# Performance work log

Hardware: AMD Instinct MI355X
Metric: run time of the kernel (lower is better)

Reference implementation:

```python
import jax, jax.numpy as jnp
import numpy as np

B, N, DIM, H, DH, P = 4, 4096, 256, 8, 64, 2
INNER = H * DH  # 512


def setup_inputs() -> dict:
    key = jax.random.key(0)
    ks = jax.random.split(key, 10)
    w = lambda k, shape: jax.random.normal(k, shape, dtype=jnp.float32) * 0.02
    return dict(
        x=jax.random.normal(ks[0], (B, N, DIM), dtype=jnp.float32),
        prev_x=jax.random.normal(ks[1], (B, N, DIM), dtype=jnp.float32),
        ln_q_g=jnp.ones((2 * DIM,), jnp.float32), ln_q_b=jnp.zeros((2 * DIM,), jnp.float32),
        ln_k_g=jnp.ones((DIM,), jnp.float32), ln_k_b=jnp.zeros((DIM,), jnp.float32),
        ln_v_g=jnp.ones((DIM,), jnp.float32), ln_v_b=jnp.zeros((DIM,), jnp.float32),
        Wq=w(ks[2], (2 * DIM, INNER)),            # to_q, bias=False
        Wk=w(ks[3], (DIM, INNER)), bk=jnp.zeros((INNER,), jnp.float32),
        Wv=w(ks[4], (DIM, INNER)), bv=jnp.zeros((INNER,), jnp.float32),
        Woff=w(ks[5], (H * P, INNER)),            # 1x1 conv == linear over channels
        boff=jax.random.uniform(ks[6], (H * P,), jnp.float32, -1.0, 1.0),
        Wout=w(ks[7], (DIM, INNER)), bout=jnp.zeros((DIM,), jnp.float32),
    )


def _ln(x, g, b):
    m = x.mean(-1, keepdims=True)
    v = ((x - m) ** 2).mean(-1, keepdims=True)
    return (x - m) * jax.lax.rsqrt(v + 1e-5) * g + b


def reference(x, prev_x, ln_q_g, ln_q_b, ln_k_g, ln_k_b, ln_v_g, ln_v_b,
              Wq, Wk, bk, Wv, bv, Woff, boff, Wout, bout):
    scale = DH ** -0.5
    # queries from cat(x, prev_x) along feature dim
    q = _ln(jnp.concatenate([x, prev_x], axis=-1), ln_q_g, ln_q_b) @ Wq  # (B,N,INNER)
    # learned per-head, per-point offsets (1x1 conv over channels)
    offsets = (q @ Woff.T + boff).reshape(B, N, H, P).transpose(0, 2, 3, 1)  # (B,H,P,N)
    # K/V from cat(x, prev_x) along batch dim -> KV length 2N per (b,h)
    kv = jnp.concatenate([x, prev_x], axis=0)  # (2B,N,DIM)
    k = (_ln(kv, ln_k_g, ln_k_b) @ Wk + bk).reshape(2, B, N, H, DH).transpose(1, 3, 4, 0, 2).reshape(B, H, DH, 2 * N)
    v = (_ln(kv, ln_v_g, ln_v_b) @ Wv + bv).reshape(2, B, N, H, DH).transpose(1, 3, 4, 0, 2).reshape(B, H, DH, 2 * N)
    # sampling positions: pos + offset, clamped, truncated to int (matches torch .long())
    pos = jnp.arange(N, dtype=jnp.float32)
    samp = jnp.clip(pos[None, None, None, :] + offsets, 0, 2 * N - 1).astype(jnp.int32)  # (B,H,P,N)
    idx = samp.transpose(0, 1, 3, 2)[:, :, None, :, :]  # (B,H,1,N,P)
    k_s = jnp.take_along_axis(k[:, :, :, None, :], idx, axis=-1)  # (B,H,DH,N,P)
    v_s = jnp.take_along_axis(v[:, :, :, None, :], idx, axis=-1)  # (B,H,DH,N,P)
    qh = q.reshape(B, N, H, DH).transpose(0, 2, 1, 3) * scale     # (B,H,N,DH)
    sim = jnp.einsum('bhnd,bhdnp->bhnp', qh, k_s)                  # (B,H,N,P)
    attn = jax.nn.softmax(sim, axis=-1)
    out = jnp.einsum('bhnp,bhdnp->bhnd', attn, v_s)                # (B,H,N,DH)
    out = out.transpose(0, 2, 1, 3).reshape(B, N, INNER) @ Wout.T + bout  # (B,N,DIM)
    return out, offsets
```

## Files before the change

kernel.cpp:

```cpp
#include <hip/hip_runtime.h>
#include <hip/hip_bf16.h>
#include <math.h>

#define B_    4
#define N_    4096
#define DIM_  256
#define H_    8
#define DH_   64
#define P_    2
#define INNER_ 512
#define BN_   (B_ * N_)
#define KVR_  (2 * BN_)

typedef short v8s  __attribute__((ext_vector_type(8)));
typedef short v4s  __attribute__((ext_vector_type(4)));
typedef float v4f  __attribute__((ext_vector_type(4)));

__device__ __forceinline__ short f2b(float x) {
    __hip_bfloat16 h = __float2bfloat16(x);
    return *reinterpret_cast<short*>(&h);
}
__device__ __forceinline__ float b2f(short s) {
    __hip_bfloat16 h = *reinterpret_cast<__hip_bfloat16*>(&s);
    return __bfloat162float(h);
}

__device__ __forceinline__ void storeC(float* p, float v) { *p = v; }
__device__ __forceinline__ void storeC(__hip_bfloat16* p, float v) { *p = __float2bfloat16(v); }

__global__ void prep_t(const float* __restrict__ W, const float* __restrict__ g,
                       const float* __restrict__ beta, const float* __restrict__ bias_in,
                       short* __restrict__ Wt, float* __restrict__ b2, int K, int N) {
    int n = blockIdx.x, t = threadIdx.x;
    float partial = 0.f;
    for (int k = t; k < K; k += 256) {
        float w = W[k * N + n];
        Wt[(size_t)n * K + k] = f2b(g[k] * w);
        partial += beta[k] * w;
    }
    __shared__ float red[256];
    red[t] = partial;
    __syncthreads();
    for (int s = 128; s > 0; s >>= 1) {
        if (t < s) red[t] += red[t + s];
        __syncthreads();
    }
    if (t == 0) b2[n] = (bias_in ? bias_in[n] : 0.f) + red[0];
}

__global__ void cast_bf16(const float* __restrict__ src, short* __restrict__ dst, int n) {
    int i = blockIdx.x * 256 + threadIdx.x;
    if (i < n) dst[i] = f2b(src[i]);
}

__global__ void wcomb_kernel(const float* __restrict__ Wq, const float* __restrict__ gq,
                             const float* __restrict__ Woff, float* __restrict__ Wcomb) {
    int k = blockIdx.x, t = threadIdx.x;
    int hp = t & 15, jg = t >> 4;
    float p = 0.f;
    for (int j = jg; j < INNER_; j += 16)
        p += Wq[k * INNER_ + j] * Woff[hp * INNER_ + j];
    __shared__ float red[16][17];
    red[jg][hp] = p;
    __syncthreads();
    if (t < 16) {
        float s = 0.f;
        for (int i = 0; i < 16; i++) s += red[i][t];
        Wcomb[k * 16 + t] = gq[k] * s;
    }
}

__global__ void bcomb_kernel(const float* __restrict__ bq2, const float* __restrict__ Woff,
                             const float* __restrict__ boff, float* __restrict__ bcomb) {
    int t = threadIdx.x;
    int hp = t & 15, jg = t >> 4;
    float p = 0.f;
    for (int j = jg; j < INNER_; j += 16)
        p += bq2[j] * Woff[hp * INNER_ + j];
    __shared__ float red[16][17];
    red[jg][hp] = p;
    __syncthreads();
    if (t < 16) {
        float s = 0.f;
        for (int i = 0; i < 16; i++) s += red[i][t];
        bcomb[t] = s + boff[t];
    }
}

__global__ __launch_bounds__(256) void norm_fused_kernel(
    const float* __restrict__ x, const float* __restrict__ p,
    const float* __restrict__ Wcomb, const float* __restrict__ bcomb,
    short* __restrict__ Aq, short* __restrict__ Akv,
    float* __restrict__ out_off, int* __restrict__ idx) {
    const int lane = threadIdx.x & 63;
    const int wv   = threadIdx.x >> 6;
    const int m0   = (blockIdx.x * 4 + wv) * 4;
    const int k8   = lane * 8;

    float4 w[8][4];
#pragma unroll
    for (int i = 0; i < 8; i++) {
        const float4* wr = (const float4*)(Wcomb + (size_t)(k8 + i) * 16);
#pragma unroll
        for (int j = 0; j < 4; j++) w[i][j] = wr[j];
    }
    const float bc = bcomb[lane & 15];

    const float* srcb = (lane < 32) ? (x + k8) : (p + k8 - DIM_);

    float4 u0 = ((const float4*)(srcb + (size_t)m0 * DIM_))[0];
    float4 u1 = ((const float4*)(srcb + (size_t)m0 * DIM_))[1];

#pragma unroll
    for (int r = 0; r < 4; r++) {
        const int m = m0 + r;
        float4 n0, n1;
        if (r < 3) {
            n0 = ((const float4*)(srcb + (size_t)(m + 1) * DIM_))[0];
            n1 = ((const float4*)(srcb + (size_t)(m + 1) * DIM_))[1];
        }
        float uv[8] = { u0.x, u0.y, u0.z, u0.w, u1.x, u1.y, u1.z, u1.w };

        float s = 0.f, q2 = 0.f;
#pragma unroll
        for (int i = 0; i < 8; i++) { s += uv[i]; q2 += uv[i] * uv[i]; }
#pragma unroll
        for (int d = 1; d <= 16; d <<= 1) {
            s  += __shfl_xor(s, d);
            q2 += __shfl_xor(q2, d);
        }
        float mean_h = s * (1.f / 256.f);
        float var_h  = q2 * (1.f / 256.f) - mean_h * mean_h;
        float rstd_h = rsqrtf(var_h + 1e-5f);
        float sf  = s  + __shfl_xor(s, 32);
        float q2f = q2 + __shfl_xor(q2, 32);
        float mean_q = sf * (1.f / 512.f);
        float var_q  = q2f * (1.f / 512.f) - mean_q * mean_q;
        float rstd_q = rsqrtf(var_q + 1e-5f);

        v8s okv;
#pragma unroll
        for (int i = 0; i < 8; i++) okv[i] = f2b((uv[i] - mean_h) * rstd_h);
        short* akvdst = Akv + ((lane < 32) ? ((size_t)m * DIM_ + k8)
                                           : ((size_t)(BN_ + m) * DIM_ + k8 - DIM_));
        *(v8s*)akvdst = okv;

        float nv[8];
        v8s oq;
#pragma unroll
        for (int i = 0; i < 8; i++) { nv[i] = (uv[i] - mean_q) * rstd_q; oq[i] = f2b(nv[i]); }
        *(v8s*)(Aq + (size_t)m * INNER_ + k8) = oq;

        float acc[16];
#pragma unroll
        for (int h = 0; h < 16; h++) acc[h] = 0.f;
#pragma unroll
        for (int i = 0; i < 8; i++) {
            float nvi = nv[i];
            acc[0]  += nvi * w[i][0].x;  acc[1]  += nvi * w[i][0].y;
            acc[2]  += nvi * w[i][0].z;  acc[3]  += nvi * w[i][0].w;
            acc[4]  += nvi * w[i][1].x;  acc[5]  += nvi * w[i][1].y;
            acc[6]  += nvi * w[i][1].z;  acc[7]  += nvi * w[i][1].w;
            acc[8]  += nvi * w[i][2].x;  acc[9]  += nvi * w[i][2].y;
            acc[10] += nvi * w[i][2].z;  acc[11] += nvi * w[i][2].w;
            acc[12] += nvi * w[i][3].x;  acc[13] += nvi * w[i][3].y;
            acc[14] += nvi * w[i][3].z;  acc[15] += nvi * w[i][3].w;
        }
        float a8[8];
#pragma unroll
        for (int j = 0; j < 8; j++) {
            float lo = acc[2 * j] + __shfl_xor(acc[2 * j], 1);
            float hi = acc[2 * j + 1] + __shfl_xor(acc[2 * j + 1], 1);
            a8[j] = (lane & 1) ? hi : lo;
        }
        float a4[4];
#pragma unroll
        for (int j = 0; j < 4; j++) {
            float lo = a8[2 * j] + __shfl_xor(a8[2 * j], 2);
            float hi = a8[2 * j + 1] + __shfl_xor(a8[2 * j + 1], 2);
            a4[j] = (lane & 2) ? hi : lo;
        }
        float a2[2];
#pragma unroll
        for (int j = 0; j < 2; j++) {
            float lo = a4[2 * j] + __shfl_xor(a4[2 * j], 4);
            float hi = a4[2 * j + 1] + __shfl_xor(a4[2 * j + 1], 4);
            a2[j] = (lane & 4) ? hi : lo;
        }
        float l1 = a2[0] + __shfl_xor(a2[0], 8);
        float h1 = a2[1] + __shfl_xor(a2[1], 8);
        float a1 = (lane & 8) ? h1 : l1;
        a1 += __shfl_xor(a1, 16);
        a1 += __shfl_xor(a1, 32);

        if (lane < 16) {
            float off = a1 + bc;
            int b = m >> 12, n = m & (N_ - 1);
            int h = lane >> 1, pp = lane & 1;
            out_off[(size_t)((b * H_ + h) * P_ + pp) * N_ + n] = off;
            float f = fminf(fmaxf((float)n + off, 0.f), (float)(2 * N_ - 1));
            idx[((size_t)(b * H_ + h) * N_ + n) * P_ + pp] = (int)f;
        }
        u0 = n0; u1 = n1;
    }
}

template <typename OT>
__global__ __launch_bounds__(256) void gemm_mfma(
    const short* __restrict__ A, const short* __restrict__ Bt,
    const float* __restrict__ bias, OT* __restrict__ C, int M, int N, int K) {
    __shared__ short As[128 * 32];
    __shared__ short Bs[128 * 32];
    const int tid  = threadIdx.x;
    const int lane = tid & 63, w = tid >> 6;
    const int wr = w >> 1, wc = w & 1;
    const int row0 = blockIdx.y * 128, col0 = blockIdx.x * 128;
    const int lm = lane & 15, g = lane >> 4;

    v4f acc[4][4];
#pragma unroll
    for (int i = 0; i < 4; i++)
#pragma unroll
        for (int j = 0; j < 4; j++) acc[i][j] = (v4f){0.f, 0.f, 0.f, 0.f};

    const int c0 = tid, c1 = tid + 256;
    const int tr0 = c0 >> 2, kg0 = (c0 & 3) ^ (tr0 & 3);
    const int tr1 = c1 >> 2, kg1 = (c1 & 3) ^ (tr1 & 3);

    for (int k0 = 0; k0 < K; k0 += 32) {
        v8s ra0 = *(const v8s*)(A  + (size_t)(row0 + tr0) * K + k0 + kg0 * 8);
        v8s ra1 = *(const v8s*)(A  + (size_t)(row0 + tr1) * K + k0 + kg1 * 8);
        v8s rb0 = *(const v8s*)(Bt + (size_t)(col0 + tr0) * K + k0 + kg0 * 8);
        v8s rb1 = *(const v8s*)(Bt + (size_t)(col0 + tr1) * K + k0 + kg1 * 8);
        __syncthreads();
        *(v8s*)(As + c0 * 8) = ra0;
        *(v8s*)(As + c1 * 8) = ra1;
        *(v8s*)(Bs + c0 * 8) = rb0;
        *(v8s*)(Bs + c1 * 8) = rb1;
        __syncthreads();

        v8s af[4], bf[4];
#pragma unroll
        for (int i = 0; i < 4; i++) {
            int m  = wr * 64 + i * 16 + lm;
            int ch = m * 4 + (g ^ (m & 3));
            af[i] = *(const v8s*)(As + ch * 8);
        }
#pragma unroll
        for (int j = 0; j < 4; j++) {
            int n  = wc * 64 + j * 16 + lm;
            int ch = n * 4 + (g ^ (n & 3));
            bf[j] = *(const v8s*)(Bs + ch * 8);
        }
#pragma unroll
        for (int i = 0; i < 4; i++)
#pragma unroll
            for (int j = 0; j < 4; j++)
                acc[i][j] = __builtin_amdgcn_mfma_f32_16x16x32_bf16(af[i], bf[j], acc[i][j], 0, 0, 0);
    }

#pragma unroll
    for (int j = 0; j < 4; j++) {
        int gc = col0 + wc * 64 + j * 16 + lm;
        float bj = bias ? bias[gc] : 0.f;
#pragma unroll
        for (int i = 0; i < 4; i++) {
            int gr = row0 + wr * 64 + i * 16 + g * 4;
#pragma unroll
            for (int r = 0; r < 4; r++)
                storeC(&C[(size_t)(gr + r) * N + gc], acc[i][j][r] + bj);
        }
    }
}

__global__ __launch_bounds__(256) void attn_kernel(
    const short* __restrict__ qb, const short* __restrict__ kvproj,
    const int* __restrict__ idx, short* __restrict__ attnout) {
    int lane = threadIdx.x & 63;
    int wv   = threadIdx.x >> 6;
    int n0 = blockIdx.x * 8 + wv * 2;
    int h = blockIdx.y, b = blockIdx.z;
    int mA = b * N_ + n0, mB = mA + 1;

    float qA = b2f(qb[(size_t)mA * INNER_ + h * DH_ + lane]) * 0.125f;
    float qB = b2f(qb[(size_t)mB * INNER_ + h * DH_ + lane]) * 0.125f;

    const int* ipA = idx + ((size_t)(b * H_ + h) * N_ + n0) * P_;
    int jA0 = ipA[0], jA1 = ipA[1], jB0 = ipA[2], jB1 = ipA[3];
    int rA0 = b * N_ + jA0 + ((jA0 >= N_) ? (BN_ - N_) : 0);
    int rA1 = b * N_ + jA1 + ((jA1 >= N_) ? (BN_ - N_) : 0);
    int rB0 = b * N_ + jB0 + ((jB0 >= N_) ? (BN_ - N_) : 0);
    int rB1 = b * N_ + jB1 + ((jB1 >= N_) ? (BN_ - N_) : 0);
    size_t oA0 = (size_t)rA0 * 1024 + h * DH_ + lane;
    size_t oA1 = (size_t)rA1 * 1024 + h * DH_ + lane;
    size_t oB0 = (size_t)rB0 * 1024 + h * DH_ + lane;
    size_t oB1 = (size_t)rB1 * 1024 + h * DH_ + lane;

    float kA0 = b2f(kvproj[oA0]),       kA1 = b2f(kvproj[oA1]);
    float kB0 = b2f(kvproj[oB0]),       kB1 = b2f(kvproj[oB1]);
    float vA0 = b2f(kvproj[oA0 + 512]), vA1 = b2f(kvproj[oA1 + 512]);
    float vB0 = b2f(kvproj[oB0 + 512]), vB1 = b2f(kvproj[oB1 + 512]);

    float sA0 = qA * kA0, sA1 = qA * kA1;
    float sB0 = qB * kB0, sB1 = qB * kB1;
    for (int d = 1; d < 64; d <<= 1) {
        sA0 += __shfl_xor(sA0, d);
        sA1 += __shfl_xor(sA1, d);
        sB0 += __shfl_xor(sB0, d);
        sB1 += __shfl_xor(sB1, d);
    }
    float mxA = fmaxf(sA0, sA1), mxB = fmaxf(sB0, sB1);
    float eA0 = __expf(sA0 - mxA), eA1 = __expf(sA1 - mxA);
    float eB0 = __expf(sB0 - mxB), eB1 = __expf(sB1 - mxB);
    float invA = 1.f / (eA0 + eA1), invB = 1.f / (eB0 + eB1);
    attnout[(size_t)mA * INNER_ + h * DH_ + lane] = f2b((eA0 * vA0 + eA1 * vA1) * invA);
    attnout[(size_t)mB * INNER_ + h * DH_ + lane] = f2b((eB0 * vB0 + eB1 * vB1) * invB);
}

extern "C" void kernel_launch(void* const* d_in, const int* in_sizes, int n_in,
                              void* d_out, int out_size, void* d_ws, size_t ws_size,
                              hipStream_t stream) {
    (void)in_sizes; (void)n_in; (void)out_size; (void)ws_size;

    const float* x      = (const float*)d_in[0];
    const float* prevx  = (const float*)d_in[1];
    const float* ln_q_g = (const float*)d_in[2];
    const float* ln_q_b = (const float*)d_in[3];
    const float* ln_k_g = (const float*)d_in[4];
    const float* ln_k_b = (const float*)d_in[5];
    const float* ln_v_g = (const float*)d_in[6];
    const float* ln_v_b = (const float*)d_in[7];
    const float* Wq     = (const float*)d_in[8];
    const float* Wk     = (const float*)d_in[9];
    const float* bk     = (const float*)d_in[10];
    const float* Wv     = (const float*)d_in[11];
    const float* bv     = (const float*)d_in[12];
    const float* Woff   = (const float*)d_in[13];
    const float* boff   = (const float*)d_in[14];
    const float* Wout   = (const float*)d_in[15];
    const float* bout   = (const float*)d_in[16];

    char* cur = (char*)d_ws;
    auto alloc = [&](size_t bytes) { char* p = cur; cur += (bytes + 255) & ~(size_t)255; return p; };
    short* Aq      = (short*)alloc((size_t)BN_ * INNER_ * 2);
    short* Akv     = (short*)alloc((size_t)KVR_ * DIM_ * 2);
    short* qb      = (short*)alloc((size_t)BN_ * INNER_ * 2);
    short* kvproj  = (short*)alloc((size_t)KVR_ * 1024 * 2);
    short* attnout = (short*)alloc((size_t)BN_ * INNER_ * 2);
    short* Wq2t    = (short*)alloc(512 * 512 * 2);
    short* Wkvt    = (short*)alloc(1024 * 256 * 2);
    short* Woutb   = (short*)alloc(256 * 512 * 2);
    float* bq2     = (float*)alloc(512 * 4);
    float* bkv     = (float*)alloc(1024 * 4);
    float* Wcomb   = (float*)alloc(512 * 16 * 4);
    float* bcomb   = (float*)alloc(16 * 4);
    int*   idxb    = (int*)alloc((size_t)BN_ * 16 * 4);

    float* out_main = (float*)d_out;
    float* out_off  = out_main + (size_t)BN_ * DIM_;

    prep_t<<<512, 256, 0, stream>>>(Wq, ln_q_g, ln_q_b, nullptr, Wq2t, bq2, 512, 512);
    prep_t<<<512, 256, 0, stream>>>(Wk, ln_k_g, ln_k_b, bk, Wkvt, bkv, 256, 512);
    prep_t<<<512, 256, 0, stream>>>(Wv, ln_v_g, ln_v_b, bv, Wkvt + 512 * 256, bkv + 512, 256, 512);
    cast_bf16<<<512, 256, 0, stream>>>(Wout, Woutb, 256 * 512);
    wcomb_kernel<<<512, 256, 0, stream>>>(Wq, ln_q_g, Woff, Wcomb);
    bcomb_kernel<<<1, 256, 0, stream>>>(bq2, Woff, boff, bcomb);

    norm_fused_kernel<<<BN_ / 16, 256, 0, stream>>>(x, prevx, Wcomb, bcomb,
                                                    Aq, Akv, out_off, idxb);

    gemm_mfma<__hip_bfloat16><<<dim3(INNER_ / 128, BN_ / 128), 256, 0, stream>>>(
        Aq, Wq2t, bq2, (__hip_bfloat16*)qb, BN_, INNER_, 512);
    gemm_mfma<__hip_bfloat16><<<dim3(1024 / 128, KVR_ / 128), 256, 0, stream>>>(
        Akv, Wkvt, bkv, (__hip_bfloat16*)kvproj, KVR_, 1024, 256);

    dim3 ga(N_ / 8, H_, B_);
    attn_kernel<<<ga, 256, 0, stream>>>(qb, kvproj, idxb, attnout);

    gemm_mfma<float><<<dim3(DIM_ / 128, BN_ / 128), 256, 0, stream>>>(
        attnout, Woutb, bout, out_main, BN_, DIM_, 512);
}
```

Before: 256.6 us.

## Use direct global-to-LDS loads, K=64 tiles, swizzled grid, LDS-staged epilogue

The GEMM now loads A/B tiles straight into LDS with global_load_lds instead of going through registers, and doubles the K step to 64 with an 8-way XOR swizzle. Blocks are remapped in groups of 8 rows for better L2 reuse. The epilogue stages accumulators in LDS per wave so each lane writes 16 contiguous outputs as vector stores instead of scattered scalar stores. The risks are the extra syncthreads in the epilogue and the lack of double-buffering, which leaves the loads exposed between barriers.

```diff
diff --git a/kernel.cpp b/kernel.cpp
--- a/kernel.cpp
+++ b/kernel.cpp
@@ -25,8 +25,23 @@
     return __bfloat162float(h);
 }
 
-__device__ __forceinline__ void storeC(float* p, float v) { *p = v; }
-__device__ __forceinline__ void storeC(__hip_bfloat16* p, float v) { *p = __float2bfloat16(v); }
+__device__ __forceinline__ void async16(const void* g, void* l) {
+    __builtin_amdgcn_global_load_lds(
+        (const __attribute__((address_space(1))) void*)g,
+        (__attribute__((address_space(3))) void*)l, 16, 0, 0);
+}
+
+__device__ __forceinline__ void storeRow(float* p, float4 f0, float4 f1, float4 f2, float4 f3) {
+    ((float4*)p)[0] = f0; ((float4*)p)[1] = f1; ((float4*)p)[2] = f2; ((float4*)p)[3] = f3;
+}
+__device__ __forceinline__ void storeRow(__hip_bfloat16* p, float4 f0, float4 f1, float4 f2, float4 f3) {
+    v8s o0, o1;
+    o0[0]=f2b(f0.x); o0[1]=f2b(f0.y); o0[2]=f2b(f0.z); o0[3]=f2b(f0.w);
+    o0[4]=f2b(f1.x); o0[5]=f2b(f1.y); o0[6]=f2b(f1.z); o0[7]=f2b(f1.w);
+    o1[0]=f2b(f2.x); o1[1]=f2b(f2.y); o1[2]=f2b(f2.z); o1[3]=f2b(f2.w);
+    o1[4]=f2b(f3.x); o1[5]=f2b(f3.y); o1[6]=f2b(f3.z); o1[7]=f2b(f3.w);
+    ((v8s*)p)[0] = o0; ((v8s*)p)[1] = o1;
+}
 
 __global__ void prep_t(const float* __restrict__ W, const float* __restrict__ g,
                        const float* __restrict__ beta, const float* __restrict__ bias_in,
@@ -209,54 +224,58 @@
 __global__ __launch_bounds__(256) void gemm_mfma(
     const short* __restrict__ A, const short* __restrict__ Bt,
     const float* __restrict__ bias, OT* __restrict__ C, int M, int N, int K) {
-    __shared__ short As[128 * 32];
-    __shared__ short Bs[128 * 32];
+    __shared__ short smem[2 * 128 * 64];
+    short* As = smem;
+    short* Bs = smem + 128 * 64;
     const int tid  = threadIdx.x;
     const int lane = tid & 63, w = tid >> 6;
     const int wr = w >> 1, wc = w & 1;
-    const int row0 = blockIdx.y * 128, col0 = blockIdx.x * 128;
     const int lm = lane & 15, g = lane >> 4;
 
+    const int nx  = gridDim.x;
+    const int lin = blockIdx.y * nx + blockIdx.x;
+    const int x8 = lin & 7, t = lin >> 3;
+    const int bx = t % nx, by = (t / nx) * 8 + x8;
+    const int row0 = by * 128, col0 = bx * 128;
+
     v4f acc[4][4];
 #pragma unroll
     for (int i = 0; i < 4; i++)
 #pragma unroll
         for (int j = 0; j < 4; j++) acc[i][j] = (v4f){0.f, 0.f, 0.f, 0.f};
 
-    const int c0 = tid, c1 = tid + 256;
-    const int tr0 = c0 >> 2, kg0 = (c0 & 3) ^ (tr0 & 3);
-    const int tr1 = c1 >> 2, kg1 = (c1 & 3) ^ (tr1 & 3);
-
-    for (int k0 = 0; k0 < K; k0 += 32) {
-        v8s ra0 = *(const v8s*)(A  + (size_t)(row0 + tr0) * K + k0 + kg0 * 8);
-        v8s ra1 = *(const v8s*)(A  + (size_t)(row0 + tr1) * K + k0 + kg1 * 8);
-        v8s rb0 = *(const v8s*)(Bt + (size_t)(col0 + tr0) * K + k0 + kg0 * 8);
-        v8s rb1 = *(const v8s*)(Bt + (size_t)(col0 + tr1) * K + k0 + kg1 * 8);
+    for (int k0 = 0; k0 < K; k0 += 64) {
         __syncthreads();
-        *(v8s*)(As + c0 * 8) = ra0;
-        *(v8s*)(As + c1 * 8) = ra1;
-        *(v8s*)(Bs + c0 * 8) = rb0;
-        *(v8s*)(Bs + c1 * 8) = rb1;
+#pragma unroll
+        for (int r = 0; r < 4; r++) {
+            int s   = tid + 256 * r;
+            int row = s >> 3, kcs = s & 7;
+            int kg  = kcs ^ (row & 7);
+            async16(A  + (size_t)(row0 + row) * K + k0 + kg * 8, (char*)As + s * 16);
+            async16(Bt + (size_t)(col0 + row) * K + k0 + kg * 8, (char*)Bs + s * 16);
+        }
         __syncthreads();
-
-        v8s af[4], bf[4];
-#pragma unroll
-        for (int i = 0; i < 4; i++) {
-            int m  = wr * 64 + i * 16 + lm;
-            int ch = m * 4 + (g ^ (m & 3));
-            af[i] = *(const v8s*)(As + ch * 8);
-        }
-#pragma unroll
-        for (int j = 0; j < 4; j++) {
-            int n  = wc * 64 + j * 16 + lm;
-            int ch = n * 4 + (g ^ (n & 3));
-            bf[j] = *(const v8s*)(Bs + ch * 8);
-        }
-#pragma unroll
-        for (int i = 0; i < 4; i++)
-#pragma unroll
-            for (int j = 0; j < 4; j++)
-                acc[i][j] = __builtin_amdgcn_mfma_f32_16x16x32_bf16(af[i], bf[j], acc[i][j], 0, 0, 0);
+#pragma unroll
+        for (int ks = 0; ks < 2; ks++) {
+            v8s af[4], bf[4];
+#pragma unroll
+            for (int i = 0; i < 4; i++) {
+                int m   = wr * 64 + i * 16 + lm;
+                int sch = m * 8 + ((ks * 4 + g) ^ (m & 7));
+                af[i] = *(const v8s*)(As + sch * 8);
+            }
+#pragma unroll
+            for (int j = 0; j < 4; j++) {
+                int n   = wc * 64 + j * 16 + lm;
+                int sch = n * 8 + ((ks * 4 + g) ^ (n & 7));
+                bf[j] = *(const v8s*)(Bs + sch * 8);
+            }
+#pragma unroll
+            for (int i = 0; i < 4; i++)
+#pragma unroll
+                for (int j = 0; j < 4; j++)
+                    acc[i][j] = __builtin_amdgcn_mfma_f32_16x16x32_bf16(af[i], bf[j], acc[i][j], 0, 0, 0);
+        }
     }
 
 #pragma unroll
@@ -264,12 +283,30 @@
         int gc = col0 + wc * 64 + j * 16 + lm;
         float bj = bias ? bias[gc] : 0.f;
 #pragma unroll
-        for (int i = 0; i < 4; i++) {
-            int gr = row0 + wr * 64 + i * 16 + g * 4;
+        for (int i = 0; i < 4; i++)
+#pragma unroll
+            for (int r = 0; r < 4; r++) acc[i][j][r] += bj;
+    }
+
+    __syncthreads();
+    float* ep = (float*)smem + w * (16 * 68);
+#pragma unroll
+    for (int i = 0; i < 4; i++) {
+#pragma unroll
+        for (int j = 0; j < 4; j++)
 #pragma unroll
             for (int r = 0; r < 4; r++)
-                storeC(&C[(size_t)(gr + r) * N + gc], acc[i][j][r] + bj);
-        }
+                ep[(g * 4 + r) * 68 + j * 16 + lm] = acc[i][j][r];
+        __syncthreads();
+        int rr = lane >> 2, cb = (lane & 3) * 16;
+        float4 f0 = *(float4*)(ep + rr * 68 + cb + 0);
+        float4 f1 = *(float4*)(ep + rr * 68 + cb + 4);
+        float4 f2 = *(float4*)(ep + rr * 68 + cb + 8);
+        float4 f3 = *(float4*)(ep + rr * 68 + cb + 12);
+        __syncthreads();
+        int grow = row0 + wr * 64 + i * 16 + rr;
+        int gcol = col0 + wc * 64 + cb;
+        storeRow(&C[(size_t)grow * N + gcol], f0, f1, f2, f3);
     }
 }
 
```

After: 246.4 us. 4.0% less time.
